# Optimization experiments

Hardware: AMD Instinct MI355X
Metric: run time of the kernel (lower is better)

Reference implementation:

```python
import jax, jax.numpy as jnp
import numpy as np

L, S, B, E, H, FF = 2048, 2048, 4, 1024, 16, 4096
HD = E // H
EPS = 1e-5


def _ln(x, g, b):
    mu = jnp.mean(x, axis=-1, keepdims=True)
    var = jnp.mean(jnp.square(x - mu), axis=-1, keepdims=True)
    return (x - mu) * jax.lax.rsqrt(var + EPS) * g + b


def _mha(xq, xk, xv, Wq, bq, Wk, bk, Wv, bv, Wo, bo, mask):
    l, bsz, e = xq.shape
    s = xk.shape[0]
    q = (xq @ Wq.T + bq).reshape(l, bsz, H, HD)
    k = (xk @ Wk.T + bk).reshape(s, bsz, H, HD)
    v = (xv @ Wv.T + bv).reshape(s, bsz, H, HD)
    scores = jnp.einsum('lbhd,sbhd->bhls', q, k) / (float(HD) ** 0.5)
    if mask is not None:
        scores = scores + mask  # broadcast (L,S) over (B,H,L,S)
    w = jax.nn.softmax(scores, axis=-1)
    out = jnp.einsum('bhls,sbhd->lbhd', w, v).reshape(l, bsz, e)
    return out @ Wo.T + bo


def setup_inputs() -> dict:
    key = jax.random.key(0)
    ks = jax.random.split(key, 32)
    sc = 0.02
    d = {
        'tgt': jax.random.normal(ks[0], (L, B, E), jnp.float32),
        'memory': jax.random.normal(ks[1], (S, B, E), jnp.float32),
        'tgt_mask': jnp.where(jnp.triu(jnp.ones((L, L), bool), k=1), -jnp.inf, 0.0).astype(jnp.float32),
    }
    def lin(i, out_d, in_d):
        return jax.random.normal(ks[i], (out_d, in_d), jnp.float32) * sc, jnp.zeros((out_d,), jnp.float32)
    for pfx, base in (('sa', 2), ('ca', 6)):
        for j, nm in enumerate(('Wq', 'Wk', 'Wv', 'Wo')):
            W, b = lin(base + j, E, E)
            d[f'{pfx}_{nm}'] = W
            d[f'{pfx}_b{nm[1]}'] = b
    d['W1'], d['b1'] = lin(10, FF, E)
    d['W2'], d['b2'] = lin(11, E, FF)
    for i, nm in enumerate(('ln1', 'ln2', 'ln3')):
        d[f'{nm}_g'] = jnp.ones((E,), jnp.float32)
        d[f'{nm}_b'] = jnp.zeros((E,), jnp.float32)
    return d


def reference(tgt, memory, tgt_mask,
              sa_Wq, sa_bq, sa_Wk, sa_bk, sa_Wv, sa_bv, sa_Wo, sa_bo,
              ca_Wq, ca_bq, ca_Wk, ca_bk, ca_Wv, ca_bv, ca_Wo, ca_bo,
              W1, b1, W2, b2,
              ln1_g, ln1_b, ln2_g, ln2_b, ln3_g, ln3_b):
    # masked self-attention + residual + norm1
    sa = _mha(tgt, tgt, tgt, sa_Wq, sa_bq, sa_Wk, sa_bk, sa_Wv, sa_bv, sa_Wo, sa_bo, tgt_mask)
    x = _ln(tgt + sa, ln1_g, ln1_b)
    # cross-attention + residual + norm2
    ca = _mha(x, memory, memory, ca_Wq, ca_bq, ca_Wk, ca_bk, ca_Wv, ca_bv, ca_Wo, ca_bo, None)
    x = _ln(x + ca, ln2_g, ln2_b)
    # FFN + residual + norm3 (dropout = identity in eval)
    ffn = jax.nn.relu(x @ W1.T + b1) @ W2.T + b2
    return _ln(x + ffn, ln3_g, ln3_b)
```

## Files before the change

### kernel.cpp

```cpp
#include <hip/hip_runtime.h>
#include <cstdint>

typedef unsigned short u16;
typedef __bf16 bf16x8 __attribute__((ext_vector_type(8)));
typedef float f32x4 __attribute__((ext_vector_type(4)));

#define L_ 2048
#define S_ 2048
#define B_ 4
#define E_ 1024
#define H_ 16
#define FF_ 4096
#define M_ (L_*B_)

#define QK_SCALE 0.18033688f

__device__ __forceinline__ unsigned f2bf(float f) {
  unsigned u = __float_as_uint(f);
  return (u + 0x7fffu + ((u >> 16) & 1u)) >> 16;
}
__device__ __forceinline__ float bflo(unsigned u){ return __uint_as_float(u << 16); }
__device__ __forceinline__ float bfhi(unsigned u){ return __uint_as_float(u & 0xffff0000u); }

struct CvtSeg { const float* src; u16* dst; int blk_end; };
struct CvtTab { CvtSeg s[6]; };

__global__ __launch_bounds__(256) void cvt_all(CvtTab t, int nseg) {
  const int blk = blockIdx.x;
  int k = 0;
  while (k < nseg - 1 && blk >= t.s[k].blk_end) k++;
  const int b0 = (k == 0) ? 0 : t.s[k-1].blk_end;
  const int off = (blk - b0) * 1024 + threadIdx.x * 4;
  float4 f = *(const float4*)(t.s[k].src + off);
  uint2 u;
  u.x = f2bf(f.x) | (f2bf(f.y) << 16);
  u.y = f2bf(f.z) | (f2bf(f.w) << 16);
  *(uint2*)(t.s[k].dst + off) = u;
}

struct GTab { u16* o[3]; const float* b[3]; float sc[3]; };

__device__ __forceinline__ void gl_lds16(const u16* g, u16* l) {
  __builtin_amdgcn_global_load_lds(
      (const __attribute__((address_space(1))) unsigned int*)g,
      (__attribute__((address_space(3))) unsigned int*)l, 16, 0, 0);
}

#define RAW_BARRIER() do { \
  asm volatile("" ::: "memory"); \
  __builtin_amdgcn_s_barrier(); \
  asm volatile("" ::: "memory"); \
} while (0)

template<int RELU, int NG>
__global__ __launch_bounds__(512, 2) void gemm256(
    const u16* __restrict__ A,
    const u16* __restrict__ Bw,
    GTab t, int K, int N)
{
  extern __shared__ __align__(16) u16 LDs[];
  const int tid  = threadIdx.x;
  const int lane = tid & 63;
  const int quad = lane >> 4;
  const int l16  = lane & 15;
  const int w    = tid >> 6;
  const int wm   = w >> 2;
  const int wn   = w & 3;
  const int bm = blockIdx.y << 8;
  const int bn = blockIdx.x << 8;

  const int grp = (NG > 1) ? ((int)blockIdx.x >> 2) : 0;
  u16* Cb = t.o[grp];
  const float* bias = t.b[grp];
  const float scale = t.sc[grp];
  const int ld = (NG > 1) ? 1024 : N;

  const int srow = (w << 4) + (lane >> 2);
  const int cg8  = ((lane & 3) ^ ((lane >> 3) & 3)) << 3;
  const u16* pa0 = A  + (size_t)(bm + srow) * K + cg8;
  const u16* pa1 = pa0 + (size_t)128 * K;
  const u16* pb0 = Bw + (size_t)(bn + srow) * K + cg8;
  const u16* pb1 = pb0 + (size_t)128 * K;
  const int wds = w << 9;

  const int swz  = (quad ^ ((l16 >> 1) & 3)) << 3;
  const int aoff = ((wm << 7) + l16) * 32 + swz;
  const int boff = 8192 + ((wn << 6) + l16) * 32 + swz;

  f32x4 acc[8][4];
  #pragma unroll
  for (int i = 0; i < 8; i++)
    #pragma unroll
    for (int j = 0; j < 4; j++)
      acc[i][j] = (f32x4){0.f, 0.f, 0.f, 0.f};

  const int nk = K >> 5;

  #pragma unroll
  for (int kt = 0; kt < 3; kt++) {
    const int sb = kt << 14;
    gl_lds16(pa0 + kt*32, LDs + sb + wds);
    gl_lds16(pa1 + kt*32, LDs + sb + 4096  + wds);
    gl_lds16(pb0 + kt*32, LDs + sb + 8192  + wds);
    gl_lds16(pb1 + kt*32, LDs + sb + 12288 + wds);
  }
  pa0 += 96; pa1 += 96; pb0 += 96; pb1 += 96;
  asm volatile("s_waitcnt vmcnt(8)" ::: "memory");
  RAW_BARRIER();

  for (int it = 0; it < nk; ++it) {
    const int rb = (it & 3) << 14;
    const int sb = ((it + 3) & 3) << 14;

    bf16x8 bfr[4], afr[4];
    #pragma unroll
    for (int nt = 0; nt < 4; nt++)
      bfr[nt] = *(const bf16x8*)(LDs + rb + boff + nt*512);
    #pragma unroll
    for (int mt = 0; mt < 4; mt++)
      afr[mt] = *(const bf16x8*)(LDs + rb + aoff + mt*512);
    gl_lds16(pa0, LDs + sb + wds);
    gl_lds16(pa1, LDs + sb + 4096 + wds);
    RAW_BARRIER();
    __builtin_amdgcn_s_setprio(1);
    #pragma unroll
    for (int mt = 0; mt < 4; mt++)
      #pragma unroll
      for (int nt = 0; nt < 4; nt++)
        acc[mt][nt] = __builtin_amdgcn_mfma_f32_16x16x32_bf16(afr[mt], bfr[nt], acc[mt][nt], 0, 0, 0);
    __builtin_amdgcn_s_setprio(0);
    RAW_BARRIER();

    #pragma unroll
    for (int mt = 0; mt < 4; mt++)
      afr[mt] = *(const bf16x8*)(LDs + rb + aoff + (4 + mt)*512);
    gl_lds16(pb0, LDs + sb + 8192  + wds);
    gl_lds16(pb1, LDs + sb + 12288 + wds);
    asm volatile("s_waitcnt vmcnt(8)" ::: "memory");
    RAW_BARRIER();
    __builtin_amdgcn_s_setprio(1);
    #pragma unroll
    for (int mt = 0; mt < 4; mt++)
      #pragma unroll
      for (int nt = 0; nt < 4; nt++)
        acc[4 + mt][nt] = __builtin_amdgcn_mfma_f32_16x16x32_bf16(afr[mt], bfr[nt], acc[4 + mt][nt], 0, 0, 0);
    __builtin_amdgcn_s_setprio(0);
    RAW_BARRIER();

    if (it + 4 < nk) { pa0 += 32; pa1 += 32; pb0 += 32; pb1 += 32; }
  }

  float bv[4];
  const int colb  = bn + (wn << 6);
  const int ocolb = (NG > 1) ? (colb & 1023) : colb;
  #pragma unroll
  for (int nt = 0; nt < 4; nt++)
    bv[nt] = bias[ocolb + nt*16 + l16];

  u16* stg = LDs + w * 4608;
  const int srd = (lane >> 3) * 72 + ((lane & 7) << 3);
  const int sc8 = (lane & 7) << 3;
  RAW_BARRIER();
  #pragma unroll
  for (int half = 0; half < 2; half++) {
    #pragma unroll
    for (int mt = 0; mt < 4; mt++)
      #pragma unroll
      for (int nt = 0; nt < 4; nt++)
        #pragma unroll
        for (int i = 0; i < 4; i++) {
          float v = (acc[half*4 + mt][nt][i] + bv[nt]) * scale;
          if (RELU) v = fmaxf(v, 0.0f);
          stg[(mt*16 + quad*4 + i)*72 + nt*16 + l16] = (u16)f2bf(v);
        }
    #pragma unroll
    for (int oct = 0; oct < 8; oct++) {
      uint4 vv = *(const uint4*)(stg + oct*576 + srd);
      u16* dst = Cb + (size_t)(bm + (wm << 7) + half*64 + oct*8 + (lane >> 3)) * ld
                    + ocolb + sc8;
      *(uint4*)dst = vv;
    }
  }
}

template<int RELU>
__global__ __launch_bounds__(512, 2) void gemm256n(
    const u16* __restrict__ A,
    const u16* __restrict__ Bw,
    const float* __restrict__ bias,
    u16* __restrict__ C,
    float scale, int K, int N)
{
  extern __shared__ __align__(16) u16 LDs[];
  const int tid  = threadIdx.x;
  const int lane = tid & 63;
  const int quad = lane >> 4;
  const int l16  = lane & 15;
  const int w    = tid >> 6;
  const int wm   = w >> 1;
  const int wn   = w & 1;

  const int bx = blockIdx.x, by = blockIdx.y;
  const int bmq = (bx << 2) + (by & 3);
  const int bnq = by >> 2;
  const int bm = bmq << 8;
  const int bn = bnq << 7;

  const int srow = (w << 4) + (lane >> 2);
  const int cg8  = ((lane & 3) ^ ((lane >> 3) & 3)) << 3;
  const u16* pa0 = A  + (size_t)(bm + srow) * K + cg8;
  const u16* pa1 = pa0 + (size_t)128 * K;
  const u16* pb0 = Bw + (size_t)(bn + srow) * K + cg8;
  const int wds = w << 9;

  const int swz  = (quad ^ ((l16 >> 1) & 3)) << 3;
  const int aoff = ((wm << 6) + l16) * 32 + swz;
  const int boff = 8192 + ((wn << 6) + l16) * 32 + swz;

  f32x4 acc[4][4];
  #pragma unroll
  for (int i = 0; i < 4; i++)
    #pragma unroll
    for (int j = 0; j < 4; j++)
      acc[i][j] = (f32x4){0.f, 0.f, 0.f, 0.f};

  const int nk = K >> 5;

  #pragma unroll
  for (int kt = 0; kt < 4; kt++) {
    const int sb = kt * 12288;
    gl_lds16(pa0 + kt*32, LDs + sb + wds);
    gl_lds16(pa1 + kt*32, LDs + sb + 4096 + wds);
    gl_lds16(pb0 + kt*32, LDs + sb + 8192 + wds);
  }
  pa0 += 128; pa1 += 128; pb0 += 128;
  asm volatile("s_waitcnt vmcnt(9)" ::: "memory");
  RAW_BARRIER();

  int rb = 0, sb = 49152;
  for (int it = 0; it < nk; ++it) {
    bf16x8 bfr[4], afr0, afr1;
    #pragma unroll
    for (int nt = 0; nt < 4; nt++)
      bfr[nt] = *(const bf16x8*)(LDs + rb + boff + nt*512);
    afr0 = *(const bf16x8*)(LDs + rb + aoff);
    afr1 = *(const bf16x8*)(LDs + rb + aoff + 512);
    gl_lds16(pa0, LDs + sb + wds);
    gl_lds16(pa1, LDs + sb + 4096 + wds);
    RAW_BARRIER();
    __builtin_amdgcn_s_setprio(1);
    #pragma unroll
    for (int nt = 0; nt < 4; nt++) {
      acc[0][nt] = __builtin_amdgcn_mfma_f32_16x16x32_bf16(afr0, bfr[nt], acc[0][nt], 0, 0, 0);
      acc[1][nt] = __builtin_amdgcn_mfma_f32_16x16x32_bf16(afr1, bfr[nt], acc[1][nt], 0, 0, 0);
    }
    __builtin_amdgcn_s_setprio(0);
    RAW_BARRIER();

    afr0 = *(const bf16x8*)(LDs + rb + aoff + 1024);
    afr1 = *(const bf16x8*)(LDs + rb + aoff + 1536);
    gl_lds16(pb0, LDs + sb + 8192 + wds);
    asm volatile("s_waitcnt vmcnt(9)" ::: "memory");
    RAW_BARRIER();
    __builtin_amdgcn_s_setprio(1);
    #pragma unroll
    for (int nt = 0; nt < 4; nt++) {
      acc[2][nt] = __builtin_amdgcn_mfma_f32_16x16x32_bf16(afr0, bfr[nt], acc[2][nt], 0, 0, 0);
      acc[3][nt] = __builtin_amdgcn_mfma_f32_16x16x32_bf16(afr1, bfr[nt], acc[3][nt], 0, 0, 0);
    }
    __builtin_amdgcn_s_setprio(0);
    RAW_BARRIER();

    if (it + 5 < nk) { pa0 += 32; pa1 += 32; pb0 += 32; }
    rb += 12288; if (rb == 61440) rb = 0;
    sb += 12288; if (sb == 61440) sb = 0;
  }

  #pragma unroll
  for (int nt = 0; nt < 4; nt++) {
    const int col = bn + (wn << 6) + nt*16 + l16;
    const float bv = bias[col];
    #pragma unroll
    for (int mt = 0; mt < 4; mt++) {
      #pragma unroll
      for (int i = 0; i < 4; i++) {
        const int row = bm + (wm << 6) + mt*16 + quad*4 + i;
        float v = (acc[mt][nt][i] + bv) * scale;
        if (RELU) v = fmaxf(v, 0.0f);
        C[(size_t)row * N + col] = (u16)f2bf(v);
      }
    }
  }
}

__global__ __launch_bounds__(256) void transpose_v(
    const u16* __restrict__ V, u16* __restrict__ Vt)
{
  __shared__ unsigned T32[64][36];
  const int t  = threadIdx.x;
  const int bh = blockIdx.y;
  const int b = bh >> 4, h = bh & 15;
  const int lblk = blockIdx.x << 6;

  {
    const int il = t >> 2;
    const int c  = (t & 3) << 4;
    const u16* src = V + ((size_t)(lblk + il) * B_ + b) * E_ + h*64 + c;
    uint4 u0 = *(const uint4*)src;
    uint4 u1 = *(const uint4*)(src + 8);
    const int g0 = (t & 3) << 1;
    const int sw = il >> 4;
    *(uint4*)&T32[il][((g0    ) ^ sw) << 2] = u0;
    *(uint4*)&T32[il][((g0 + 1) ^ sw) << 2] = u1;
  }
  __syncthreads();

  {
    const int d  = t >> 2;
    const int ls = (t & 3) << 4;
    const int dp = d >> 1, hi = d & 1;
    const int pc = dp ^ ((t & 3) << 2);
    unsigned o[16];
    #pragma unroll
    for (int j = 0; j < 16; j++) {
      unsigned wv = T32[ls + j][pc];
      o[j] = hi ? (wv >> 16) : (wv & 0xffffu);
    }
    uint4 v0, v1;
    v0.x = o[0]  | (o[1]  << 16); v0.y = o[2]  | (o[3]  << 16);
    v0.z = o[4]  | (o[5]  << 16); v0.w = o[6]  | (o[7]  << 16);
    v1.x = o[8]  | (o[9]  << 16); v1.y = o[10] | (o[11] << 16);
    v1.z = o[12] | (o[13] << 16); v1.w = o[14] | (o[15] << 16);
    u16* dst = Vt + (size_t)(bh*64 + d) * S_ + lblk + ls;
    *(uint4*)dst       = v0;
    *(uint4*)(dst + 8) = v1;
  }
}

template<int CAUSAL>
__global__ __launch_bounds__(256, 4) void attn_mfma(
    const u16* __restrict__ Q,
    const u16* __restrict__ Kg,
    const u16* __restrict__ Vt,
    u16* __restrict__ O,
    int Skv)
{
  __shared__ __align__(16) u16 Tile[16384];
  const int tid  = threadIdx.x;
  const int lane = tid & 63;
  const int w    = tid >> 6;
  const int l16  = lane & 15;
  const int quad = lane >> 4;
  const int bh = blockIdx.x;
  const int b = bh >> 4, h = bh & 15;
  const int y = blockIdx.y;
  const int q0 = (CAUSAL ? ((y < 8) ? (15 - 2*y) : (2*y - 16)) : y) << 7;
  const int wq = q0 + w*32;

  bf16x8 qf[2][2];
  #pragma unroll
  for (int h2 = 0; h2 < 2; h2++) {
    const size_t qoff = ((size_t)(wq + h2*16 + l16) * B_ + b) * E_ + h*64;
    qf[h2][0] = *(const bf16x8*)(Q + qoff + quad*8);
    qf[h2][1] = *(const bf16x8*)(Q + qoff + 32 + quad*8);
  }

  const uint4 ones_u = {0x3F803F80u, 0x3F803F80u, 0x3F803F80u, 0x3F803F80u};
  const bf16x8 ones = *(const bf16x8*)&ones_u;

  f32x4 oacc[2][4];
  #pragma unroll
  for (int h2 = 0; h2 < 2; h2++)
    #pragma unroll
    for (int i = 0; i < 4; i++) oacc[h2][i] = (f32x4){0.f,0.f,0.f,0.f};
  f32x4 lsacc[2];
  lsacc[0] = (f32x4){0.f,0.f,0.f,0.f};
  lsacc[1] = (f32x4){0.f,0.f,0.f,0.f};

  const int lrow = lane >> 3;
  const int lchunk = (lane & 7) ^ lrow;
  const u16* kp = Kg + ((size_t)(16*w + lrow) * B_ + b) * E_ + h*64 + lchunk*8;
  const u16* vp = Vt + (size_t)(bh*64 + 16*w + lrow) * Skv + lchunk*8;
  const size_t kRow8 = (size_t)8 * B_ * E_;
  const size_t kTile = (size_t)64 * B_ * E_;
  u16* ldsK = Tile + w*1024;
  u16* ldsV = Tile + 4096 + w*1024;

  const int pbase = 8192 + w*2048;
  int aKV[2], aW[4];
  #pragma unroll
  for (int kh = 0; kh < 2; kh++)
    aKV[kh] = l16*64 + (((kh*4 + quad) ^ (l16 & 7)) << 3);
  #pragma unroll
  for (int st = 0; st < 4; st++)
    aW[st] = pbase + l16*64 +
             ((((st*2) + (quad >> 1)) ^ (l16 & 7)) << 3) + ((quad & 1) << 2);

  const int send = CAUSAL ? (q0 + 128) : Skv;
  for (int s0 = 0; s0 < send; s0 += 64) {
    __syncthreads();
    gl_lds16(kp,         ldsK);
    gl_lds16(kp + kRow8, ldsK + 512);
    gl_lds16(vp,         ldsV);
    gl_lds16(vp + 8*Skv, ldsV + 512);
    kp += kTile; vp += 64;
    __syncthreads();

    if (CAUSAL && s0 >= wq + 32) continue;

    f32x4 sacc[2][4];
    #pragma unroll
    for (int h2 = 0; h2 < 2; h2++)
      #pragma unroll
      for (int st = 0; st < 4; st++) sacc[h2][st] = (f32x4){0.f,0.f,0.f,0.f};
    #pragma unroll
    for (int kh = 0; kh < 2; kh++)
      #pragma unroll
      for (int st = 0; st < 4; st++) {
        bf16x8 kf = *(const bf16x8*)(Tile + aKV[kh] + st*1024);
        sacc[0][st] = __builtin_amdgcn_mfma_f32_16x16x32_bf16(kf, qf[0][kh], sacc[0][st], 0, 0, 0);
        sacc[1][st] = __builtin_amdgcn_mfma_f32_16x16x32_bf16(kf, qf[1][kh], sacc[1][st], 0, 0, 0);
      }

    #pragma unroll
    for (int h2 = 0; h2 < 2; h2++) {
      float p[16];
      #pragma unroll
      for (int st = 0; st < 4; st++)
        #pragma unroll
        for (int r = 0; r < 4; r++) p[st*4+r] = sacc[h2][st][r];
      if (CAUSAL && s0 + 63 > wq + h2*16) {
        const int qa = wq + h2*16 + l16;
        #pragma unroll
        for (int st = 0; st < 4; st++)
          #pragma unroll
          for (int r = 0; r < 4; r++)
            if (s0 + st*16 + quad*4 + r > qa) p[st*4+r] = -3e38f;
      }
      #pragma unroll
      for (int i = 0; i < 16; i++) p[i] = __builtin_amdgcn_exp2f(p[i]);

      #pragma unroll
      for (int st = 0; st < 4; st++) {
        uint2 d;
        d.x = __builtin_amdgcn_perm(__float_as_uint(p[st*4+1]), __float_as_uint(p[st*4+0]), 0x07060302u);
        d.y = __builtin_amdgcn_perm(__float_as_uint(p[st*4+3]), __float_as_uint(p[st*4+2]), 0x07060302u);
        *(uint2*)(Tile + aW[st] + h2*1024) = d;
      }
    }

    #pragma unroll
    for (int kh = 0; kh < 2; kh++) {
      bf16x8 pf[2];
      #pragma unroll
      for (int h2 = 0; h2 < 2; h2++)
        pf[h2] = *(const bf16x8*)(Tile + pbase + h2*1024 + aKV[kh]);
      lsacc[0] = __builtin_amdgcn_mfma_f32_16x16x32_bf16(pf[0], ones, lsacc[0], 0, 0, 0);
      lsacc[1] = __builtin_amdgcn_mfma_f32_16x16x32_bf16(pf[1], ones, lsacc[1], 0, 0, 0);
      #pragma unroll
      for (int dt = 0; dt < 4; dt++) {
        bf16x8 vf = *(const bf16x8*)(Tile + 4096 + aKV[kh] + dt*1024);
        #pragma unroll
        for (int h2 = 0; h2 < 2; h2++)
          oacc[h2][dt] = __builtin_amdgcn_mfma_f32_16x16x32_bf16(pf[h2], vf, oacc[h2][dt], 0, 0, 0);
      }
    }
  }

  #pragma unroll
  for (int h2 = 0; h2 < 2; h2++) {
    #pragma unroll
    for (int r = 0; r < 4; r++) {
      const float inv = 1.0f / lsacc[h2][r];
      const int qg = wq + h2*16 + quad*4 + r;
      const size_t orow = ((size_t)qg * B_ + b) * E_ + h*64;
      #pragma unroll
      for (int dt = 0; dt < 4; dt++)
        O[orow + dt*16 + l16] = (u16)f2bf(oacc[h2][dt][r] * inv);
    }
  }
}

template<int RF32>
__global__ __launch_bounds__(256) void add_ln(
    const u16* __restrict__ X,
    const float* __restrict__ Rf, const u16* __restrict__ Rb,
    const float* __restrict__ g, const float* __restrict__ be,
    float* __restrict__ outF, u16* __restrict__ outB)
{
  const int row = blockIdx.x;
  const int tid = threadIdx.x;
  const size_t base = (size_t)row * E_;
  uint2 xu = *(const uint2*)(X + base + tid*4);
  float x0 = bflo(xu.x), x1 = bfhi(xu.x), x2 = bflo(xu.y), x3 = bfhi(xu.y);
  float r0, r1, r2, r3;
  if (RF32) {
    float4 rv = *(const float4*)(Rf + base + tid*4);
    r0 = rv.x; r1 = rv.y; r2 = rv.z; r3 = rv.w;
  } else {
    uint2 ru = *(const uint2*)(Rb + base + tid*4);
    r0 = bflo(ru.x); r1 = bfhi(ru.x); r2 = bflo(ru.y); r3 = bfhi(ru.y);
  }
  const float v0 = x0 + r0, v1 = x1 + r1, v2 = x2 + r2, v3 = x3 + r3;
  float s  = v0 + v1 + v2 + v3;
  float s2 = v0*v0 + v1*v1 + v2*v2 + v3*v3;
  #pragma unroll
  for (int off = 32; off >= 1; off >>= 1) {
    s  += __shfl_down(s,  off);
    s2 += __shfl_down(s2, off);
  }
  __shared__ float ps[4], ps2[4];
  const int wv = tid >> 6, lane = tid & 63;
  if (lane == 0) { ps[wv] = s; ps2[wv] = s2; }
  __syncthreads();
  const float ts  = ps[0] + ps[1] + ps[2] + ps[3];
  const float ts2 = ps2[0] + ps2[1] + ps2[2] + ps2[3];
  const float mu  = ts * (1.0f / E_);
  const float var = ts2 * (1.0f / E_) - mu * mu;
  const float rsq = rsqrtf(var + 1e-5f);
  float4 gv = *(const float4*)(g  + tid*4);
  float4 bv = *(const float4*)(be + tid*4);
  const float o0 = (v0 - mu) * rsq * gv.x + bv.x;
  const float o1 = (v1 - mu) * rsq * gv.y + bv.y;
  const float o2 = (v2 - mu) * rsq * gv.z + bv.z;
  const float o3 = (v3 - mu) * rsq * gv.w + bv.w;
  if (outF) {
    float4 ov; ov.x = o0; ov.y = o1; ov.z = o2; ov.w = o3;
    *(float4*)(outF + base + tid*4) = ov;
  }
  if (outB) {
    uint2 u;
    u.x = f2bf(o0) | (f2bf(o1) << 16);
    u.y = f2bf(o2) | (f2bf(o3) << 16);
    *(uint2*)(outB + base + tid*4) = u;
  }
}

extern "C" void kernel_launch(void* const* d_in, const int* in_sizes, int n_in,
                              void* d_out, int out_size, void* d_ws, size_t ws_size,
                              hipStream_t stream) {
  (void)in_sizes; (void)n_in; (void)out_size; (void)ws_size;
  const float* tgt  = (const float*)d_in[0];
  const float* mem  = (const float*)d_in[1];
  const float* saWq = (const float*)d_in[3];  const float* sabq = (const float*)d_in[4];
  const float* saWk = (const float*)d_in[5];  const float* sabk = (const float*)d_in[6];
  const float* saWv = (const float*)d_in[7];  const float* sabv = (const float*)d_in[8];
  const float* saWo = (const float*)d_in[9];  const float* sabo = (const float*)d_in[10];
  const float* caWq = (const float*)d_in[11]; const float* cabq = (const float*)d_in[12];
  const float* caWk = (const float*)d_in[13]; const float* cabk = (const float*)d_in[14];
  const float* caWv = (const float*)d_in[15]; const float* cabv = (const float*)d_in[16];
  const float* caWo = (const float*)d_in[17]; const float* cabo = (const float*)d_in[18];
  const float* W1   = (const float*)d_in[19]; const float* b1   = (const float*)d_in[20];
  const float* W2   = (const float*)d_in[21]; const float* b2   = (const float*)d_in[22];
  const float* ln1g = (const float*)d_in[23]; const float* ln1b = (const float*)d_in[24];
  const float* ln2g = (const float*)d_in[25]; const float* ln2b = (const float*)d_in[26];
  const float* ln3g = (const float*)d_in[27]; const float* ln3b = (const float*)d_in[28];
  float* out = (float*)d_out;

  static bool attr_done = false;
  if (!attr_done) {
    (void)hipFuncSetAttribute(reinterpret_cast<const void*>(&gemm256<0,3>),
                              hipFuncAttributeMaxDynamicSharedMemorySize, 131072);
    (void)hipFuncSetAttribute(reinterpret_cast<const void*>(&gemm256<0,2>),
                              hipFuncAttributeMaxDynamicSharedMemorySize, 131072);
    (void)hipFuncSetAttribute(reinterpret_cast<const void*>(&gemm256<1,1>),
                              hipFuncAttributeMaxDynamicSharedMemorySize, 131072);
    (void)hipFuncSetAttribute(reinterpret_cast<const void*>(&gemm256n<0>),
                              hipFuncAttributeMaxDynamicSharedMemorySize, 122880);
    attr_done = true;
  }

  char* wsp = (char*)d_ws;
  const size_t MB16 = (size_t)16 * 1024 * 1024;
  u16* A  = (u16*)(wsp + 0 * MB16);
  u16* Cq = (u16*)(wsp + 1 * MB16);
  u16* Bm = (u16*)(wsp + 2 * MB16);
  u16* Dk = (u16*)(wsp + 3 * MB16);
  u16* Ev = (u16*)(wsp + 4 * MB16);
  u16* Ff = (u16*)(wsp + 5 * MB16);
  u16* wS = (u16*)(wsp + 6 * MB16);
  u16* hb = Cq;
  const int MEG = 1024 * 1024;

  dim3 blk(256);
  dim3 blk512(512);
  dim3 gN1(8, 32);
  dim3 gQKV256(12, 32);
  dim3 gKV256(8, 32);
  dim3 gFF256(16, 32);
  dim3 ga(B_*H_, L_/128);
  dim3 gt(S_/64, B_*H_);

  {
    CvtTab t{};
    t.s[0] = {tgt,  A,        8192};
    t.s[1] = {mem,  Bm,       16384};
    t.s[2] = {saWq, wS,       17408};
    t.s[3] = {saWk, wS + MEG,   18432};
    t.s[4] = {saWv, wS + 2*MEG, 19456};
    t.s[5] = {saWo, wS + 3*MEG, 20480};
    cvt_all<<<20480, blk, 0, stream>>>(t, 6);
  }

  {
    GTab t{};
    t.o[0]=Cq; t.o[1]=Dk; t.o[2]=Ev;
    t.b[0]=sabq; t.b[1]=sabk; t.b[2]=sabv;
    t.sc[0]=QK_SCALE; t.sc[1]=1.f; t.sc[2]=1.f;
    gemm256<0,3><<<gQKV256, blk512, 131072, stream>>>(A, wS, t, E_, 3*E_);
  }
  transpose_v<<<gt, blk, 0, stream>>>(Ev, Ff);
  attn_mfma<1><<<ga, blk, 0, stream>>>(Cq, Dk, Ff, Cq, S_);
  gemm256n<0><<<gN1, blk512, 122880, stream>>>(Cq, wS + 3*MEG, sabo, Ff, 1.f, E_, E_);
  add_ln<1><<<M_, blk, 0, stream>>>(Ff, tgt, nullptr, ln1g, ln1b, nullptr, A);

  {
    CvtTab t{};
    t.s[0] = {caWq, wS,        1024};
    t.s[1] = {caWk, wS + MEG,    2048};
    t.s[2] = {caWv, wS + 2*MEG,  3072};
    t.s[3] = {caWo, wS + 3*MEG,  4096};
    cvt_all<<<4096, blk, 0, stream>>>(t, 4);
  }

  gemm256n<0><<<gN1, blk512, 122880, stream>>>(A, wS, cabq, Cq, QK_SCALE, E_, E_);
  {
    GTab t{};
    t.o[0]=Dk; t.o[1]=Ev; t.o[2]=Ev;
    t.b[0]=cabk; t.b[1]=cabv; t.b[2]=cabv;
    t.sc[0]=1.f; t.sc[1]=1.f; t.sc[2]=1.f;
    gemm256<0,2><<<gKV256, blk512, 131072, stream>>>(Bm, wS + MEG, t, E_, 2*E_);
  }
  transpose_v<<<gt, blk, 0, stream>>>(Ev, Ff);
  attn_mfma<0><<<ga, blk, 0, stream>>>(Cq, Dk, Ff, Cq, S_);
  gemm256n<0><<<gN1, blk512, 122880, stream>>>(Cq, wS + 3*MEG, cabo, Ff, 1.f, E_, E_);
  add_ln<0><<<M_, blk, 0, stream>>>(Ff, nullptr, A, ln2g, ln2b, nullptr, A);

  {
    CvtTab t{};
    t.s[0] = {W1, wS, 4096};
    cvt_all<<<4096, blk, 0, stream>>>(t, 1);
  }
  {
    GTab t{};
    t.o[0]=hb; t.o[1]=hb; t.o[2]=hb;
    t.b[0]=b1; t.b[1]=b1; t.b[2]=b1;
    t.sc[0]=1.f; t.sc[1]=1.f; t.sc[2]=1.f;
    gemm256<1,1><<<gFF256, blk512, 131072, stream>>>(A, wS, t, E_, FF_);
  }
  {
    CvtTab t{};
    t.s[0] = {W2, wS, 4096};
    cvt_all<<<4096, blk, 0, stream>>>(t, 1);
  }
  gemm256n<0><<<gN1, blk512, 122880, stream>>>(hb, wS, b2, Ff, 1.f, FF_, E_);
  add_ln<0><<<M_, blk, 0, stream>>>(Ff, nullptr, A, ln3g, ln3b, out, nullptr);
}
```

Before: 717.1 us.

## Double-buffer attention K/V tiles and remap GEMM block order

```diff
diff --git a/kernel.cpp b/kernel.cpp
--- a/kernel.cpp
+++ b/kernel.cpp
@@ -66,10 +66,15 @@
   const int w    = tid >> 6;
   const int wm   = w >> 2;
   const int wn   = w & 3;
-  const int bm = blockIdx.y << 8;
-  const int bn = blockIdx.x << 8;
-
-  const int grp = (NG > 1) ? ((int)blockIdx.x >> 2) : 0;
+
+  const int lid = (int)(blockIdx.y * gridDim.x + blockIdx.x);
+  const int loc = lid >> 3;
+  const int bmq = ((lid & 7) << 2) + (loc & 3);
+  const int bnq = loc >> 2;
+  const int bm = bmq << 8;
+  const int bn = bnq << 8;
+
+  const int grp = (NG > 1) ? (bnq >> 2) : 0;
   u16* Cb = t.o[grp];
   const float* bias = t.b[grp];
   const float scale = t.sc[grp];
@@ -345,7 +350,7 @@
     u16* __restrict__ O,
     int Skv)
 {
-  __shared__ __align__(16) u16 Tile[16384];
+  __shared__ __align__(16) u16 Tile[24576];
   const int tid  = threadIdx.x;
   const int lane = tid & 63;
   const int w    = tid >> 6;
@@ -383,10 +388,8 @@
   const u16* vp = Vt + (size_t)(bh*64 + 16*w + lrow) * Skv + lchunk*8;
   const size_t kRow8 = (size_t)8 * B_ * E_;
   const size_t kTile = (size_t)64 * B_ * E_;
-  u16* ldsK = Tile + w*1024;
-  u16* ldsV = Tile + 4096 + w*1024;
-
-  const int pbase = 8192 + w*2048;
+
+  const int pbase = 16384 + w*2048;
   int aKV[2], aW[4];
   #pragma unroll
   for (int kh = 0; kh < 2; kh++)
@@ -397,74 +400,89 @@
              ((((st*2) + (quad >> 1)) ^ (l16 & 7)) << 3) + ((quad & 1) << 2);
 
   const int send = CAUSAL ? (q0 + 128) : Skv;
+
+  gl_lds16(kp,         Tile + w*1024);
+  gl_lds16(kp + kRow8, Tile + w*1024 + 512);
+  gl_lds16(vp,         Tile + 8192 + w*1024);
+  gl_lds16(vp + 8*Skv, Tile + 8192 + w*1024 + 512);
+  kp += kTile; vp += 64;
+
+  int cur = 0;
   for (int s0 = 0; s0 < send; s0 += 64) {
-    __syncthreads();
-    gl_lds16(kp,         ldsK);
-    gl_lds16(kp + kRow8, ldsK + 512);
-    gl_lds16(vp,         ldsV);
-    gl_lds16(vp + 8*Skv, ldsV + 512);
-    kp += kTile; vp += 64;
-    __syncthreads();
-
-    if (CAUSAL && s0 >= wq + 32) continue;
-
-    f32x4 sacc[2][4];
-    #pragma unroll
-    for (int h2 = 0; h2 < 2; h2++)
-      #pragma unroll
-      for (int st = 0; st < 4; st++) sacc[h2][st] = (f32x4){0.f,0.f,0.f,0.f};
-    #pragma unroll
-    for (int kh = 0; kh < 2; kh++)
-      #pragma unroll
-      for (int st = 0; st < 4; st++) {
-        bf16x8 kf = *(const bf16x8*)(Tile + aKV[kh] + st*1024);
-        sacc[0][st] = __builtin_amdgcn_mfma_f32_16x16x32_bf16(kf, qf[0][kh], sacc[0][st], 0, 0, 0);
-        sacc[1][st] = __builtin_amdgcn_mfma_f32_16x16x32_bf16(kf, qf[1][kh], sacc[1][st], 0, 0, 0);
-      }
-
-    #pragma unroll
-    for (int h2 = 0; h2 < 2; h2++) {
-      float p[16];
-      #pragma unroll
-      for (int st = 0; st < 4; st++)
-        #pragma unroll
-        for (int r = 0; r < 4; r++) p[st*4+r] = sacc[h2][st][r];
-      if (CAUSAL && s0 + 63 > wq + h2*16) {
-        const int qa = wq + h2*16 + l16;
+    RAW_BARRIER();
+    const int stg = (cur ^ 1) << 12;
+    gl_lds16(kp,         Tile + stg + w*1024);
+    gl_lds16(kp + kRow8, Tile + stg + w*1024 + 512);
+    gl_lds16(vp,         Tile + 8192 + stg + w*1024);
+    gl_lds16(vp + 8*Skv, Tile + 8192 + stg + w*1024 + 512);
+    if (s0 + 128 < send) { kp += kTile; vp += 64; }
+    asm volatile("s_waitcnt vmcnt(4)" ::: "memory");
+    RAW_BARRIER();
+
+    if (!(CAUSAL && s0 >= wq + 32)) {
+      const int rk = cur << 12;
+      const int rv = 8192 + (cur << 12);
+
+      f32x4 sacc[2][4];
+      #pragma unroll
+      for (int h2 = 0; h2 < 2; h2++)
+        #pragma unroll
+        for (int st = 0; st < 4; st++) sacc[h2][st] = (f32x4){0.f,0.f,0.f,0.f};
+      #pragma unroll
+      for (int kh = 0; kh < 2; kh++)
+        #pragma unroll
+        for (int st = 0; st < 4; st++) {
+          bf16x8 kf = *(const bf16x8*)(Tile + rk + aKV[kh] + st*1024);
+          sacc[0][st] = __builtin_amdgcn_mfma_f32_16x16x32_bf16(kf, qf[0][kh], sacc[0][st], 0, 0, 0);
+          sacc[1][st] = __builtin_amdgcn_mfma_f32_16x16x32_bf16(kf, qf[1][kh], sacc[1][st], 0, 0, 0);
+        }
+
+      #pragma unroll
+      for (int h2 = 0; h2 < 2; h2++) {
+        float p[16];
         #pragma unroll
         for (int st = 0; st < 4; st++)
           #pragma unroll
-          for (int r = 0; r < 4; r++)
-            if (s0 + st*16 + quad*4 + r > qa) p[st*4+r] = -3e38f;
+          for (int r = 0; r < 4; r++) p[st*4+r] = sacc[h2][st][r];
+        if (CAUSAL && s0 + 63 > wq + h2*16) {
+          const int qa = wq + h2*16 + l16;
+          #pragma unroll
+          for (int st = 0; st < 4; st++)
+            #pragma unroll
+            for (int r = 0; r < 4; r++)
+              if (s0 + st*16 + quad*4 + r > qa) p[st*4+r] = -3e38f;
+        }
+        #pragma unroll
+        for (int i = 0; i < 16; i++) p[i] = __builtin_amdgcn_exp2f(p[i]);
+
+        #pragma unroll
+        for (int st = 0; st < 4; st++) {
+          uint2 d;
+          d.x = __builtin_amdgcn_perm(__float_as_uint(p[st*4+1]), __float_as_uint(p[st*4+0]), 0x07060302u);
+          d.y = __builtin_amdgcn_perm(__float_as_uint(p[st*4+3]), __float_as_uint(p[st*4+2]), 0x07060302u);
+          *(uint2*)(Tile + aW[st] + h2*1024) = d;
+        }
       }
-      #pragma unroll
-      for (int i = 0; i < 16; i++) p[i] = __builtin_amdgcn_exp2f(p[i]);
-
-      #pragma unroll
-      for (int st = 0; st < 4; st++) {
-        uint2 d;
-        d.x = __builtin_amdgcn_perm(__float_as_uint(p[st*4+1]), __float_as_uint(p[st*4+0]), 0x07060302u);
-        d.y = __builtin_amdgcn_perm(__float_as_uint(p[st*4+3]), __float_as_uint(p[st*4+2]), 0x07060302u);
-        *(uint2*)(Tile + aW[st] + h2*1024) = d;
+
+      #pragma unroll
+      for (int kh = 0; kh < 2; kh++) {
+        bf16x8 pf[2];
+        #pragma unroll
+        for (int h2 = 0; h2 < 2; h2++)
+          pf[h2] = *(const bf16x8*)(Tile + pbase + h2*1024 + aKV[kh]);
+        lsacc[0] = __builtin_amdgcn_mfma_f32_16x16x32_bf16(pf[0], ones, lsacc[0], 0, 0, 0);
+        lsacc[1] = __builtin_amdgcn_mfma_f32_16x16x32_bf16(pf[1], ones, lsacc[1], 0, 0, 0);
+        #pragma unroll
+        for (int dt = 0; dt < 4; dt++) {
+          bf16x8 vf = *(const bf16x8*)(Tile + rv + aKV[kh] + dt*1024);
+          #pragma unroll
+          for (int h2 = 0; h2 < 2; h2++)
+            oacc[h2][dt] = __builtin_amdgcn_mfma_f32_16x16x32_bf16(pf[h2], vf, oacc[h2][dt], 0, 0, 0);
+        }
       }
     }
 
-    #pragma unroll
-    for (int kh = 0; kh < 2; kh++) {
-      bf16x8 pf[2];
-      #pragma unroll
-      for (int h2 = 0; h2 < 2; h2++)
-        pf[h2] = *(const bf16x8*)(Tile + pbase + h2*1024 + aKV[kh]);
-      lsacc[0] = __builtin_amdgcn_mfma_f32_16x16x32_bf16(pf[0], ones, lsacc[0], 0, 0, 0);
-      lsacc[1] = __builtin_amdgcn_mfma_f32_16x16x32_bf16(pf[1], ones, lsacc[1], 0, 0, 0);
-      #pragma unroll
-      for (int dt = 0; dt < 4; dt++) {
-        bf16x8 vf = *(const bf16x8*)(Tile + 4096 + aKV[kh] + dt*1024);
-        #pragma unroll
-        for (int h2 = 0; h2 < 2; h2++)
-          oacc[h2][dt] = __builtin_amdgcn_mfma_f32_16x16x32_bf16(pf[h2], vf, oacc[h2][dt], 0, 0, 0);
-      }
-    }
+    cur ^= 1;
   }
 
   #pragma unroll
```

Measured after the change: 750.5 us. +4.6%, slower.
